# Performance work log

Measured on AMD Instinct MI355X. Metric: run time of the kernel, lower is better.

The kernel has to match this reference:

```python
import jax, jax.numpy as jnp
import numpy as np
import math

NUM_HEADS = 8
WINDOW_SIZE = 1025
GLOBAL_TOKENS = 512  # effectively min(4, GLOBAL_TOKENS) indices are used, as in the torch code


def setup_inputs() -> dict:
    key = jax.random.key(0)
    k0, k1, k2 = jax.random.split(key, 3)
    B, C, H, W = 2, 256, 64, 64
    x = jax.random.normal(k0, (B, C, H, W), dtype=jnp.float32)
    # proj1: Linear(C, 3C); proj2: Linear(C, C). Stored as [in, out] matrices.
    w1 = jax.random.normal(k1, (C, 3 * C), dtype=jnp.float32) * 0.02
    b1 = jnp.zeros((3 * C,), dtype=jnp.float32)
    w2 = jax.random.normal(k2, (C, C), dtype=jnp.float32) * 0.02
    b2 = jnp.zeros((C,), dtype=jnp.float32)
    return {"x": x, "w1": w1, "b1": b1, "w2": w2, "b2": b2}


def _longformer_bias(L, W, window_size, global_tokens, dtype):
    # band: |i - j| <= window_size // 2  (matches start/end loop in torch code)
    i = jnp.arange(L)
    band = jnp.abs(i[:, None] - i[None, :]) <= (window_size // 2)
    gidx = [0, W - 1, L - W, L - 1][:global_tokens]
    g = jnp.zeros((L,), dtype=bool).at[jnp.array(gidx)].set(True)
    mask = band | g[:, None] | g[None, :]
    return jnp.where(mask, jnp.array(0.0, dtype), jnp.array(-jnp.inf, dtype))


def reference(x, w1, b1, w2, b2):
    B, C, H, W = x.shape
    L = H * W
    hd = C // NUM_HEADS
    # b c h w -> b (h w) c
    xt = x.reshape(B, C, L).transpose(0, 2, 1)
    qkv = xt @ w1 + b1  # [B, L, 3C]
    # 'b L (C H K)' with K=3, H=heads: last dim factors as (head_dim, heads, 3)
    qkv = qkv.reshape(B, L, hd, NUM_HEADS, 3).transpose(4, 0, 3, 1, 2)  # [3, B, Hh, L, hd]
    q, k, v = qkv[0], qkv[1], qkv[2]
    bias = _longformer_bias(L, W, WINDOW_SIZE, GLOBAL_TOKENS, x.dtype)
    scale = math.sqrt(hd)
    attn = jnp.einsum('bhqc,bhkc->bhqk', q, k) / scale + bias
    attn = jax.nn.softmax(attn, axis=-1)
    o = jnp.einsum('bhqk,bhkc->bhqc', attn, v)  # [B, Hh, L, hd]
    # 'b H (h w) C -> b h w (C H)': channel index = c*num_heads + head
    o = o.transpose(0, 2, 3, 1).reshape(B, H, W, hd * NUM_HEADS)
    out = o @ w2 + b2  # [B, H, W, C]
    return out.transpose(0, 3, 1, 2)  # b h w C -> b C h w
```

## Files before the change

kernel.cpp:

```cpp
#include <hip/hip_runtime.h>
#include <hip/hip_bf16.h>

#define BB 2
#define CC 256
#define HEADS 8
#define HD 32
#define LL 4096
#define HALF_WIN 512

using short8  = __attribute__((ext_vector_type(8))) short;
using short4v = __attribute__((ext_vector_type(4))) short;
using float4v = __attribute__((ext_vector_type(4))) float;

__device__ __forceinline__ ushort f2bf(float x) {
    uint u = __float_as_uint(x);
    u += 0x7fff + ((u >> 16) & 1);
    return (ushort)(u >> 16);
}
__device__ __forceinline__ float ubf(ushort u) {
    return __uint_as_float((uint)u << 16);
}
__device__ __forceinline__ uint pk2bf(float a, float b) {
#if __has_builtin(__builtin_amdgcn_cvt_pk_bf16_f32)
    typedef __bf16 v2bf __attribute__((ext_vector_type(2)));
    union { v2bf v; uint u; } cv;
    cv.v = __builtin_amdgcn_cvt_pk_bf16_f32(a, b);
    return cv.u;
#else
    return (uint)f2bf(a) | ((uint)f2bf(b) << 16);
#endif
}
__device__ __forceinline__ float rexp2(float x) {
#if __has_builtin(__builtin_amdgcn_exp2f)
    return __builtin_amdgcn_exp2f(x);
#else
    return exp2f(x);
#endif
}

#define QSCALE 0.25503485f

__global__ __launch_bounds__(256) void wt_kernel(const float* __restrict__ w1,
                                                 const float* __restrict__ w2,
                                                 ushort* __restrict__ w1t,
                                                 ushort* __restrict__ w2t) {
    __shared__ float tl[16][17];
    const int tx = threadIdx.x & 15, ty = threadIdx.x >> 4;
    const int ci0 = blockIdx.x * 16;
    const int y = blockIdx.y;
    if (y < 48) {
        int j0 = y * 16;
        tl[ty][tx] = w1[(size_t)(ci0 + ty) * 768 + j0 + tx];
        __syncthreads();
        w1t[(size_t)(j0 + ty) * CC + ci0 + tx] = f2bf(tl[tx][ty]);
    } else {
        int co0 = (y - 48) * 16;
        tl[ty][tx] = w2[(size_t)(ci0 + ty) * CC + co0 + tx];
        __syncthreads();
        w2t[(size_t)(co0 + ty) * CC + ci0 + tx] = f2bf(tl[tx][ty]);
    }
}

__global__ __launch_bounds__(256) void qkv_kernel(const float* __restrict__ x,
                                                  const ushort* __restrict__ w1t,
                                                  const float* __restrict__ b1,
                                                  ushort* __restrict__ qb,
                                                  ushort* __restrict__ kb,
                                                  ushort* __restrict__ vt) {
    __shared__ __align__(16) ushort xs[32 * 264];
    const int dg = blockIdx.x;
    const int l0 = blockIdx.y * 32;
    const int b  = blockIdx.z;
    const int t  = threadIdx.x;
    const int w  = t >> 6, ln = t & 63, c = ln & 15, g = ln >> 4;

    {
        const int l  = t & 31;
        const int cG = (t >> 5) * 4;
#pragma unroll
        for (int p = 0; p < 8; p++) {
            int c0 = p * 32 + cG;
            float a0 = x[((size_t)b * CC + c0 + 0) * LL + l0 + l];
            float a1 = x[((size_t)b * CC + c0 + 1) * LL + l0 + l];
            float a2 = x[((size_t)b * CC + c0 + 2) * LL + l0 + l];
            float a3 = x[((size_t)b * CC + c0 + 3) * LL + l0 + l];
            uint2 u;
            u.x = pk2bf(a0, a1);
            u.y = pk2bf(a2, a3);
            *(uint2*)&xs[l * 264 + c0] = u;
        }
    }
    __syncthreads();

    const int jbase = dg * 192 + w * 48;
    float4v acc[3][2] = {};
#pragma unroll
    for (int ks = 0; ks < 8; ks++) {
        short8 af[3], bfr[2];
#pragma unroll
        for (int jt = 0; jt < 3; jt++)
            af[jt] = *(const short8*)(w1t + (size_t)(jbase + jt * 16 + c) * CC + ks * 32 + g * 8);
#pragma unroll
        for (int lt = 0; lt < 2; lt++)
            bfr[lt] = *(const short8*)&xs[(lt * 16 + c) * 264 + ks * 32 + g * 8];
#pragma unroll
        for (int jt = 0; jt < 3; jt++)
#pragma unroll
            for (int lt = 0; lt < 2; lt++)
                acc[jt][lt] = __builtin_amdgcn_mfma_f32_16x16x32_bf16(af[jt], bfr[lt], acc[jt][lt], 0, 0, 0);
    }
    __syncthreads();

    ushort* qs  = xs;
    ushort* ksm = xs + 32 * 72;
    ushort* vs  = xs + 2 * 32 * 72;

#pragma unroll
    for (int jt = 0; jt < 3; jt++) {
#pragma unroll
        for (int r = 0; r < 4; r++) {
            int j = jbase + jt * 16 + g * 4 + r;
            float bias = b1[j];
            int t3 = j % 3, h = (j / 3) & 7, dl = (j / 24) & 7;
            int slot = h * 8 + dl;
            float v0 = acc[jt][0][r] + bias;
            float v1 = acc[jt][1][r] + bias;
            if (t3 == 0) { v0 *= QSCALE; v1 *= QSCALE; }
            uint u01 = pk2bf(v0, v1);
            ushort* dst = (t3 == 0) ? qs : (t3 == 1) ? ksm : vs;
            int stride = (t3 == 2) ? 74 : 72;
            dst[c * stride + slot]        = (ushort)u01;
            dst[(16 + c) * stride + slot] = (ushort)(u01 >> 16);
        }
    }
    __syncthreads();

    {
        const int l = t & 31;
        const int h = t >> 5;
        size_t rowq = (((size_t)(b * 8 + h) * 4 + dg) * LL + l0 + l) * 8;
        *(short8*)(qb + rowq) = *(const short8*)&qs[l * 72 + h * 8];
        *(short8*)(kb + rowq) = *(const short8*)&ksm[l * 72 + h * 8];
#pragma unroll
        for (int p = 0; p < 8; p++) {
            int hd = p * 8 + h;
            vt[((size_t)(b * 8 + (hd >> 3)) * HD + dg * 8 + (hd & 7)) * LL + l0 + l] = vs[l * 74 + hd];
        }
    }
}

__device__ __forceinline__ int gcol_of(int tt) {
    return (tt == 0) ? 0 : (tt == 3) ? 63 : (tt == 252) ? LL - 64 : (tt == 255) ? LL - 1 : -1;
}

__global__ __launch_bounds__(256) void attn_kernel(const ushort* __restrict__ qb,
                                                   const ushort* __restrict__ kb,
                                                   const ushort* __restrict__ vt,
                                                   ushort* __restrict__ obuf,
                                                   float* __restrict__ gpart) {
    __shared__ __align__(16) char smem[27648];
    const int n = blockIdx.x;
    const int t = threadIdx.x;

    if (n < 256) {
        float* qs = (float*)smem;
        float* sc = qs + 128;
        const int bh = ((n & 7) << 1) | ((n >> 3) & 1);
        const int ch = n >> 4;
        const int gidx[4] = {0, 63, LL - 64, LL - 1};

        if (t < 128) {
            int r = t >> 5, dd = t & 31;
            int i = gidx[r];
            qs[r * 32 + dd] = ubf(qb[(((size_t)bh * 4 + (dd >> 3)) * LL + i) * 8 + (dd & 7)]);
        }
        __syncthreads();

        const int j = ch * 256 + t;
        float dot[4] = {};
#pragma unroll
        for (int s = 0; s < 4; s++) {
            const short8 kf = *(const short8*)(kb + (((size_t)bh * 4 + s) * LL + j) * 8);
#pragma unroll
            for (int e = 0; e < 8; e++) {
                float kv = ubf((ushort)kf[e]);
#pragma unroll
                for (int r = 0; r < 4; r++) dot[r] += qs[r * 32 + s * 8 + e] * kv;
            }
        }
#pragma unroll
        for (int r = 0; r < 4; r++) sc[r * 256 + t] = rexp2(dot[r]);
        __syncthreads();

        const int w = t >> 6, ln = t & 63;
        float den = sc[w * 256 + ln] + sc[w * 256 + ln + 64] +
                    sc[w * 256 + ln + 128] + sc[w * 256 + ln + 192];
#pragma unroll
        for (int o = 1; o < 64; o <<= 1) den += __shfl_xor(den, o);

        const int dd = ln & 31, half = ln >> 5;
        float acc = 0.f;
        const ushort* vrow = vt + ((size_t)bh * HD + dd) * LL + ch * 256 + half * 128;
#pragma unroll
        for (int q8 = 0; q8 < 16; q8++) {
            const short8 v8 = *(const short8*)(vrow + q8 * 8);
#pragma unroll
            for (int e = 0; e < 8; e++) acc += sc[w * 256 + half * 128 + q8 * 8 + e] * ubf((ushort)v8[e]);
        }
        acc += __shfl_xor(acc, 32);

        float* gp = gpart + (((size_t)bh * 16 + ch) * 4 + w) * 33;
        if (ln < 32) gp[dd] = acc;
        if (ln == 0) gp[32] = den;
        return;
    }

    ushort* pshare = (ushort*)smem;
    float*  cbuf   = (float*)smem;
    const int nb = n - 256;
    const int bh = ((nb & 7) << 1) | ((nb >> 3) & 1);
    const int it = nb >> 4;
    const int i0 = it * 64;
    const int w  = t >> 6;
    const int ln = t & 63;
    const int c  = ln & 15;
    const int g  = ln >> 4;

    const size_t slab = ((size_t)bh * 4 + g) * LL;

    short8 qf[4];
#pragma unroll
    for (int s = 0; s < 4; s++)
        qf[s] = *(const short8*)(qb + (slab + i0 + s * 16 + c) * 8);

    float4v o0[4], o1[4];
#pragma unroll
    for (int s = 0; s < 4; s++) {
#pragma unroll
        for (int r = 0; r < 4; r++) { o0[s][r] = 0.f; o1[s][r] = 0.f; }
    }
    float dsum[4] = {0.f, 0.f, 0.f, 0.f};

    int t0 = it * 4 - 32; if (t0 < 0) t0 = 0;
    int t1 = it * 4 + 35; if (t1 > 255) t1 = 255;
    int tf0 = it * 4 - 28; if (tf0 < 0) tf0 = 0;
    int tf1 = it * 4 + 31; if (tf1 > 255) tf1 = 255;

    int ml[12], nm = 0;
    for (int tt = t0; tt < tf0; tt++) ml[nm++] = tt;
    for (int tt = tf1 + 1; tt <= t1; tt++) ml[nm++] = tt;
    const int gt[4] = {0, 3, 252, 255};
#pragma unroll
    for (int e = 0; e < 4; e++)
        if (gt[e] < t0 || gt[e] > t1) ml[nm++] = gt[e];

    const ushort* vb = vt + (size_t)bh * HD * LL;
    ushort* wbb = pshare + w * 4 * 576;

    const int npair_f = (tf1 - tf0 + 1) >> 1;
    const int qq = npair_f >> 2, rem = npair_f & 3;
    const int mstart = w * qq + (w < rem ? w : rem);
    const int mcount = qq + (w < rem ? 1 : 0);
    const int tfs = tf0 + 2 * mstart;

    const ushort* kp  = kb + (slab + (size_t)(tfs * 16 + c)) * 8;
    const ushort* vp0 = vb + (size_t)c * LL + tfs * 16 + g * 8;
    const ushort* vp1 = vp0 + 16 * LL;

    short8 kfA, kfB, v0f, v1f;
    if (mcount > 0) {
        kfA = *(const short8*)kp;
        kfB = *(const short8*)(kp + 128);
        v0f = *(const short8*)vp0;
        v1f = *(const short8*)vp1;
    }
    for (int m = 0; m < mcount; m++) {
        const int adv = (m + 1 < mcount) ? 1 : 0;
        const ushort* kp2  = kp  + adv * 256;
        const ushort* vp02 = vp0 + adv * 32;
        const ushort* vp12 = vp1 + adv * 32;
        const short8 kfA2 = *(const short8*)kp2;
        const short8 kfB2 = *(const short8*)(kp2 + 128);
        const short8 v0f2 = *(const short8*)vp02;
        const short8 v1f2 = *(const short8*)vp12;

        float4v zero = {0.f, 0.f, 0.f, 0.f};
#pragma unroll
        for (int s = 0; s < 4; s++) {
            float4v sA = __builtin_amdgcn_mfma_f32_16x16x32_bf16(kfA, qf[s], zero, 0, 0, 0);
            float4v sB = __builtin_amdgcn_mfma_f32_16x16x32_bf16(kfB, qf[s], zero, 0, 0, 0);
            float pA[4], pB[4];
#pragma unroll
            for (int r = 0; r < 4; r++) { pA[r] = rexp2(sA[r]); dsum[s] += pA[r]; }
#pragma unroll
            for (int r = 0; r < 4; r++) { pB[r] = rexp2(sB[r]); dsum[s] += pB[r]; }
            uint2 ua, ub2;
            ua.x  = pk2bf(pA[0], pA[1]);
            ua.y  = pk2bf(pA[2], pA[3]);
            ub2.x = pk2bf(pB[0], pB[1]);
            ub2.y = pk2bf(pB[2], pB[3]);
            ushort* wb = wbb + s * 576;
            *(uint2*)&wb[c * 36 + 4 * g]      = ua;
            *(uint2*)&wb[c * 36 + 16 + 4 * g] = ub2;
        }
#pragma unroll
        for (int s = 0; s < 4; s++) {
            const ushort* wb = wbb + s * 576;
            union { short8 s8; short4v s4[2]; } pu;
            pu.s4[0] = *(const short4v*)&wb[c * 36 + 8 * g];
            pu.s4[1] = *(const short4v*)&wb[c * 36 + 8 * g + 4];
            o0[s] = __builtin_amdgcn_mfma_f32_16x16x32_bf16(pu.s8, v0f, o0[s], 0, 0, 0);
            o1[s] = __builtin_amdgcn_mfma_f32_16x16x32_bf16(pu.s8, v1f, o1[s], 0, 0, 0);
        }
        kfA = kfA2; kfB = kfB2; v0f = v0f2; v1f = v1f2;
        kp = kp2; vp0 = vp02; vp1 = vp12;
    }

    for (int p = 0; p < (nm >> 1); p++) {
        if ((p & 3) != w) continue;
        const int tA = ml[2 * p], tB = ml[2 * p + 1];
        const int gA = gcol_of(tA), gB = gcol_of(tB);
        const short8 mkA = *(const short8*)(kb + (slab + (size_t)(tA * 16 + c)) * 8);
        const short8 mkB = *(const short8*)(kb + (slab + (size_t)(tB * 16 + c)) * 8);
        const int jv = (g < 2) ? tA * 16 + g * 8 : tB * 16 + (g - 2) * 8;
        const short8 mv0 = *(const short8*)(vb + (size_t)c * LL + jv);
        const short8 mv1 = *(const short8*)(vb + (size_t)(16 + c) * LL + jv);
        float4v zero = {0.f, 0.f, 0.f, 0.f};
#pragma unroll
        for (int s = 0; s < 4; s++) {
            const int i = i0 + s * 16 + c;
            float4v sA = __builtin_amdgcn_mfma_f32_16x16x32_bf16(mkA, qf[s], zero, 0, 0, 0);
            float4v sB = __builtin_amdgcn_mfma_f32_16x16x32_bf16(mkB, qf[s], zero, 0, 0, 0);
            float pA[4], pB[4];
#pragma unroll
            for (int r = 0; r < 4; r++) {
                int j = tA * 16 + g * 4 + r;
                bool ok = ((unsigned)(i - j + HALF_WIN) <= 2u * HALF_WIN) | (j == gA);
                pA[r] = ok ? rexp2(sA[r]) : 0.f;
                dsum[s] += pA[r];
            }
#pragma unroll
            for (int r = 0; r < 4; r++) {
                int j = tB * 16 + g * 4 + r;
                bool ok = ((unsigned)(i - j + HALF_WIN) <= 2u * HALF_WIN) | (j == gB);
                pB[r] = ok ? rexp2(sB[r]) : 0.f;
                dsum[s] += pB[r];
            }
            uint2 ua, ub2;
            ua.x  = pk2bf(pA[0], pA[1]);
            ua.y  = pk2bf(pA[2], pA[3]);
            ub2.x = pk2bf(pB[0], pB[1]);
            ub2.y = pk2bf(pB[2], pB[3]);
            ushort* wb = wbb + s * 576;
            *(uint2*)&wb[c * 36 + 4 * g]      = ua;
            *(uint2*)&wb[c * 36 + 16 + 4 * g] = ub2;
        }
#pragma unroll
        for (int s = 0; s < 4; s++) {
            const ushort* wb = wbb + s * 576;
            union { short8 s8; short4v s4[2]; } pu;
            pu.s4[0] = *(const short4v*)&wb[c * 36 + 8 * g];
            pu.s4[1] = *(const short4v*)&wb[c * 36 + 8 * g + 4];
            o0[s] = __builtin_amdgcn_mfma_f32_16x16x32_bf16(pu.s8, mv0, o0[s], 0, 0, 0);
            o1[s] = __builtin_amdgcn_mfma_f32_16x16x32_bf16(pu.s8, mv1, o1[s], 0, 0, 0);
        }
    }

    __syncthreads();
#pragma unroll
    for (int s = 0; s < 4; s++) {
        if (s == w) continue;
        float* cb = &cbuf[((s * 3 + ((w < s) ? w : w - 1)) * 64 + ln) * 9];
#pragma unroll
        for (int r = 0; r < 4; r++) { cb[r] = o0[s][r]; cb[4 + r] = o1[s][r]; }
        cb[8] = dsum[s];
    }
    __syncthreads();

    float4v O0 = o0[w], O1 = o1[w];
    float ds = dsum[w];
#pragma unroll
    for (int k = 0; k < 3; k++) {
        const float* cb = &cbuf[((w * 3 + k) * 64 + ln) * 9];
#pragma unroll
        for (int r = 0; r < 4; r++) { O0[r] += cb[r]; O1[r] += cb[4 + r]; }
        ds += cb[8];
    }

    ds += __shfl_xor(ds, 16);
    ds += __shfl_xor(ds, 32);

    const int b = bh >> 3, hh = bh & 7;
#pragma unroll
    for (int r = 0; r < 4; r++) {
        float dn = __shfl(ds, g * 4 + r);
        float inv = 1.0f / dn;
        int irow = i0 + w * 16 + g * 4 + r;
        size_t rowb = ((size_t)b * LL + irow) * CC;
        obuf[rowb + (size_t)c * 8 + hh]        = f2bf(O0[r] * inv);
        obuf[rowb + (size_t)(16 + c) * 8 + hh] = f2bf(O1[r] * inv);
    }
}

__global__ __launch_bounds__(128) void attn_global_combine(const float* __restrict__ gpart,
                                                           ushort* __restrict__ obuf) {
    const int bh = blockIdx.x;
    const int t  = threadIdx.x;
    const int r  = t >> 5, dd = t & 31;
    const int gidx[4] = {0, 63, LL - 64, LL - 1};
    float pv = 0.f, den = 0.f;
#pragma unroll
    for (int ch = 0; ch < 16; ch++) {
        const float* gp = gpart + (((size_t)bh * 16 + ch) * 4 + r) * 33;
        pv  += gp[dd];
        den += gp[32];
    }
    const int b = bh >> 3, hh = bh & 7, i = gidx[r];
    obuf[((size_t)b * LL + i) * CC + dd * 8 + hh] = f2bf(pv / den);
}

__global__ __launch_bounds__(256) void proj_kernel(const ushort* __restrict__ obuf,
                                                   const ushort* __restrict__ w2t,
                                                   const float* __restrict__ b2,
                                                   float* __restrict__ out) {
    const int co0 = blockIdx.x * 16;
    const int w   = threadIdx.x >> 6;
    const int l0  = blockIdx.y * 128 + (w >> 1) * 64;
    const int nfb = (w & 1) * 2;
    const int b   = blockIdx.z;
    const int ln  = threadIdx.x & 63;
    const int c   = ln & 15, g = ln >> 4;

    float4v acc[2] = {};
    const ushort* arow = w2t + (size_t)(co0 + c) * CC + g * 8;
    const ushort* brow = obuf + ((size_t)b * LL + l0 + c) * CC + g * 8;
#pragma unroll
    for (int ks = 0; ks < 8; ks++) {
        const short8 af = *(const short8*)(arow + ks * 32);
#pragma unroll
        for (int k = 0; k < 2; k++) {
            const short8 bf = *(const short8*)(brow + (size_t)(nfb + k) * 16 * CC + ks * 32);
            acc[k] = __builtin_amdgcn_mfma_f32_16x16x32_bf16(af, bf, acc[k], 0, 0, 0);
        }
    }
#pragma unroll
    for (int k = 0; k < 2; k++) {
#pragma unroll
        for (int r = 0; r < 4; r++) {
            int co = co0 + g * 4 + r;
            int l  = l0 + (nfb + k) * 16 + c;
            out[((size_t)b * CC + co) * LL + l] = acc[k][r] + b2[co];
        }
    }
}

extern "C" void kernel_launch(void* const* d_in, const int* in_sizes, int n_in,
                              void* d_out, int out_size, void* d_ws, size_t ws_size,
                              hipStream_t stream) {
    const float* x  = (const float*)d_in[0];
    const float* w1 = (const float*)d_in[1];
    const float* b1 = (const float*)d_in[2];
    const float* w2 = (const float*)d_in[3];
    const float* b2 = (const float*)d_in[4];
    float* out = (float*)d_out;

    const size_t QKE = (size_t)BB * HEADS * LL * HD;
    const size_t OBE = (size_t)BB * LL * CC;
    ushort* qb  = (ushort*)d_ws;
    ushort* kb  = qb + QKE;
    ushort* vt  = kb + QKE;
    ushort* ob  = vt + QKE;
    float*  gp  = (float*)(ob + OBE);
    ushort* w2t = (ushort*)(gp + 16 * 16 * 4 * 33);
    ushort* w1t = w2t + CC * CC;

    wt_kernel<<<dim3(16, 64), 256, 0, stream>>>(w1, w2, w1t, w2t);
    qkv_kernel<<<dim3(4, 128, 2), 256, 0, stream>>>(x, w1t, b1, qb, kb, vt);
    attn_kernel<<<dim3(1280), 256, 0, stream>>>(qb, kb, vt, ob, gp);
    attn_global_combine<<<dim3(16), 128, 0, stream>>>(gp, ob);
    proj_kernel<<<dim3(16, 32, 2), 256, 0, stream>>>(ob, w2t, b2, out);
}
```

Before: 138.5 us.

## Fuse all stages into one persistent kernel with atomic grid barriers

Merges the weight transpose, QKV projection, attention, global-token combine and output projection into one persistent kernel of 512 blocks. Each stage loops over its former grid, and stages are separated by atomic-counter grid barriers; a memset resets the counters each call. This removes the launch gaps between kernels, but it relies on all 512 blocks being co-resident (launch_bounds 256,2) to avoid deadlock. Each barrier also serializes the stages, so a slow block in one stage holds up every block before the next.

```diff
diff --git a/kernel.cpp b/kernel.cpp
--- a/kernel.cpp
+++ b/kernel.cpp
@@ -7,6 +7,7 @@
 #define HD 32
 #define LL 4096
 #define HALF_WIN 512
+#define NBLK 512u
 
 using short8  = __attribute__((ext_vector_type(8))) short;
 using short4v = __attribute__((ext_vector_type(4))) short;
@@ -40,127 +41,143 @@
 
 #define QSCALE 0.25503485f
 
-__global__ __launch_bounds__(256) void wt_kernel(const float* __restrict__ w1,
-                                                 const float* __restrict__ w2,
-                                                 ushort* __restrict__ w1t,
-                                                 ushort* __restrict__ w2t) {
-    __shared__ float tl[16][17];
-    const int tx = threadIdx.x & 15, ty = threadIdx.x >> 4;
-    const int ci0 = blockIdx.x * 16;
-    const int y = blockIdx.y;
-    if (y < 48) {
-        int j0 = y * 16;
-        tl[ty][tx] = w1[(size_t)(ci0 + ty) * 768 + j0 + tx];
-        __syncthreads();
-        w1t[(size_t)(j0 + ty) * CC + ci0 + tx] = f2bf(tl[tx][ty]);
-    } else {
-        int co0 = (y - 48) * 16;
-        tl[ty][tx] = w2[(size_t)(ci0 + ty) * CC + co0 + tx];
-        __syncthreads();
-        w2t[(size_t)(co0 + ty) * CC + ci0 + tx] = f2bf(tl[tx][ty]);
-    }
-}
-
-__global__ __launch_bounds__(256) void qkv_kernel(const float* __restrict__ x,
-                                                  const ushort* __restrict__ w1t,
-                                                  const float* __restrict__ b1,
-                                                  ushort* __restrict__ qb,
-                                                  ushort* __restrict__ kb,
-                                                  ushort* __restrict__ vt) {
-    __shared__ __align__(16) ushort xs[32 * 264];
-    const int dg = blockIdx.x;
-    const int l0 = blockIdx.y * 32;
-    const int b  = blockIdx.z;
-    const int t  = threadIdx.x;
-    const int w  = t >> 6, ln = t & 63, c = ln & 15, g = ln >> 4;
-
-    {
-        const int l  = t & 31;
-        const int cG = (t >> 5) * 4;
-#pragma unroll
-        for (int p = 0; p < 8; p++) {
-            int c0 = p * 32 + cG;
-            float a0 = x[((size_t)b * CC + c0 + 0) * LL + l0 + l];
-            float a1 = x[((size_t)b * CC + c0 + 1) * LL + l0 + l];
-            float a2 = x[((size_t)b * CC + c0 + 2) * LL + l0 + l];
-            float a3 = x[((size_t)b * CC + c0 + 3) * LL + l0 + l];
-            uint2 u;
-            u.x = pk2bf(a0, a1);
-            u.y = pk2bf(a2, a3);
-            *(uint2*)&xs[l * 264 + c0] = u;
-        }
-    }
-    __syncthreads();
-
-    const int jbase = dg * 192 + w * 48;
-    float4v acc[3][2] = {};
-#pragma unroll
-    for (int ks = 0; ks < 8; ks++) {
-        short8 af[3], bfr[2];
-#pragma unroll
-        for (int jt = 0; jt < 3; jt++)
-            af[jt] = *(const short8*)(w1t + (size_t)(jbase + jt * 16 + c) * CC + ks * 32 + g * 8);
-#pragma unroll
-        for (int lt = 0; lt < 2; lt++)
-            bfr[lt] = *(const short8*)&xs[(lt * 16 + c) * 264 + ks * 32 + g * 8];
-#pragma unroll
-        for (int jt = 0; jt < 3; jt++)
-#pragma unroll
-            for (int lt = 0; lt < 2; lt++)
-                acc[jt][lt] = __builtin_amdgcn_mfma_f32_16x16x32_bf16(af[jt], bfr[lt], acc[jt][lt], 0, 0, 0);
-    }
-    __syncthreads();
-
-    ushort* qs  = xs;
-    ushort* ksm = xs + 32 * 72;
-    ushort* vs  = xs + 2 * 32 * 72;
-
-#pragma unroll
-    for (int jt = 0; jt < 3; jt++) {
-#pragma unroll
-        for (int r = 0; r < 4; r++) {
-            int j = jbase + jt * 16 + g * 4 + r;
-            float bias = b1[j];
-            int t3 = j % 3, h = (j / 3) & 7, dl = (j / 24) & 7;
-            int slot = h * 8 + dl;
-            float v0 = acc[jt][0][r] + bias;
-            float v1 = acc[jt][1][r] + bias;
-            if (t3 == 0) { v0 *= QSCALE; v1 *= QSCALE; }
-            uint u01 = pk2bf(v0, v1);
-            ushort* dst = (t3 == 0) ? qs : (t3 == 1) ? ksm : vs;
-            int stride = (t3 == 2) ? 74 : 72;
-            dst[c * stride + slot]        = (ushort)u01;
-            dst[(16 + c) * stride + slot] = (ushort)(u01 >> 16);
-        }
-    }
-    __syncthreads();
-
-    {
-        const int l = t & 31;
-        const int h = t >> 5;
-        size_t rowq = (((size_t)(b * 8 + h) * 4 + dg) * LL + l0 + l) * 8;
-        *(short8*)(qb + rowq) = *(const short8*)&qs[l * 72 + h * 8];
-        *(short8*)(kb + rowq) = *(const short8*)&ksm[l * 72 + h * 8];
-#pragma unroll
-        for (int p = 0; p < 8; p++) {
-            int hd = p * 8 + h;
-            vt[((size_t)(b * 8 + (hd >> 3)) * HD + dg * 8 + (hd & 7)) * LL + l0 + l] = vs[l * 74 + hd];
-        }
-    }
-}
-
 __device__ __forceinline__ int gcol_of(int tt) {
     return (tt == 0) ? 0 : (tt == 3) ? 63 : (tt == 252) ? LL - 64 : (tt == 255) ? LL - 1 : -1;
 }
 
-__global__ __launch_bounds__(256) void attn_kernel(const ushort* __restrict__ qb,
-                                                   const ushort* __restrict__ kb,
-                                                   const ushort* __restrict__ vt,
-                                                   ushort* __restrict__ obuf,
-                                                   float* __restrict__ gpart) {
+__device__ __forceinline__ void gbar(uint* ctr, int t) {
+    __syncthreads();
+    __threadfence();
+    if (t == 0) {
+        atomicAdd(ctr, 1u);
+        while (atomicAdd(ctr, 0u) < NBLK) __builtin_amdgcn_s_sleep(8);
+    }
+    __syncthreads();
+    __threadfence();
+}
+
+__global__ __launch_bounds__(256, 2) void mega_kernel(
+        const float* __restrict__ x,
+        const float* __restrict__ w1,
+        const float* __restrict__ b1,
+        const float* __restrict__ w2,
+        const float* __restrict__ b2,
+        float* __restrict__ out,
+        ushort* __restrict__ qb,
+        ushort* __restrict__ kb,
+        ushort* __restrict__ vt,
+        ushort* __restrict__ obuf,
+        float* __restrict__ gpart,
+        ushort* __restrict__ w2t,
+        ushort* __restrict__ w1t,
+        uint* __restrict__ bar) {
     __shared__ __align__(16) char smem[27648];
     const int n = blockIdx.x;
     const int t = threadIdx.x;
+
+    for (int jb = n; jb < 1024; jb += 512) {
+        float* tl = (float*)smem;
+        const int tx = t & 15, ty = t >> 4;
+        const int ci0 = (jb & 15) * 16;
+        const int y = jb >> 4;
+        if (y < 48) {
+            int j0 = y * 16;
+            tl[ty * 17 + tx] = w1[(size_t)(ci0 + ty) * 768 + j0 + tx];
+            __syncthreads();
+            w1t[(size_t)(j0 + ty) * CC + ci0 + tx] = f2bf(tl[tx * 17 + ty]);
+        } else {
+            int co0 = (y - 48) * 16;
+            tl[ty * 17 + tx] = w2[(size_t)(ci0 + ty) * CC + co0 + tx];
+            __syncthreads();
+            w2t[(size_t)(co0 + ty) * CC + ci0 + tx] = f2bf(tl[tx * 17 + ty]);
+        }
+        __syncthreads();
+    }
+    gbar(bar + 0, t);
+
+    for (int jb = n; jb < 1024; jb += 512) {
+        ushort* xs = (ushort*)smem;
+        const int dg = jb & 3;
+        const int l0 = ((jb >> 2) & 127) * 32;
+        const int b  = jb >> 9;
+        const int w  = t >> 6, ln = t & 63, c = ln & 15, g = ln >> 4;
+
+        {
+            const int l  = t & 31;
+            const int cG = (t >> 5) * 4;
+#pragma unroll
+            for (int p = 0; p < 8; p++) {
+                int c0 = p * 32 + cG;
+                float a0 = x[((size_t)b * CC + c0 + 0) * LL + l0 + l];
+                float a1 = x[((size_t)b * CC + c0 + 1) * LL + l0 + l];
+                float a2 = x[((size_t)b * CC + c0 + 2) * LL + l0 + l];
+                float a3 = x[((size_t)b * CC + c0 + 3) * LL + l0 + l];
+                uint2 u;
+                u.x = pk2bf(a0, a1);
+                u.y = pk2bf(a2, a3);
+                *(uint2*)&xs[l * 264 + c0] = u;
+            }
+        }
+        __syncthreads();
+
+        const int jbase = dg * 192 + w * 48;
+        float4v acc[3][2] = {};
+#pragma unroll
+        for (int ks = 0; ks < 8; ks++) {
+            short8 af[3], bfr[2];
+#pragma unroll
+            for (int jt = 0; jt < 3; jt++)
+                af[jt] = *(const short8*)(w1t + (size_t)(jbase + jt * 16 + c) * CC + ks * 32 + g * 8);
+#pragma unroll
+            for (int lt = 0; lt < 2; lt++)
+                bfr[lt] = *(const short8*)&xs[(lt * 16 + c) * 264 + ks * 32 + g * 8];
+#pragma unroll
+            for (int jt = 0; jt < 3; jt++)
+#pragma unroll
+                for (int lt = 0; lt < 2; lt++)
+                    acc[jt][lt] = __builtin_amdgcn_mfma_f32_16x16x32_bf16(af[jt], bfr[lt], acc[jt][lt], 0, 0, 0);
+        }
+        __syncthreads();
+
+        ushort* qs  = xs;
+        ushort* ksm = xs + 32 * 72;
+        ushort* vs  = xs + 2 * 32 * 72;
+
+#pragma unroll
+        for (int jt = 0; jt < 3; jt++) {
+#pragma unroll
+            for (int r = 0; r < 4; r++) {
+                int j = jbase + jt * 16 + g * 4 + r;
+                float bias = b1[j];
+                int t3 = j % 3, h = (j / 3) & 7, dl = (j / 24) & 7;
+                int slot = h * 8 + dl;
+                float v0 = acc[jt][0][r] + bias;
+                float v1 = acc[jt][1][r] + bias;
+                if (t3 == 0) { v0 *= QSCALE; v1 *= QSCALE; }
+                uint u01 = pk2bf(v0, v1);
+                ushort* dst = (t3 == 0) ? qs : (t3 == 1) ? ksm : vs;
+                int stride = (t3 == 2) ? 74 : 72;
+                dst[c * stride + slot]        = (ushort)u01;
+                dst[(16 + c) * stride + slot] = (ushort)(u01 >> 16);
+            }
+        }
+        __syncthreads();
+
+        {
+            const int l = t & 31;
+            const int h = t >> 5;
+            size_t rowq = (((size_t)(b * 8 + h) * 4 + dg) * LL + l0 + l) * 8;
+            *(short8*)(qb + rowq) = *(const short8*)&qs[l * 72 + h * 8];
+            *(short8*)(kb + rowq) = *(const short8*)&ksm[l * 72 + h * 8];
+#pragma unroll
+            for (int p = 0; p < 8; p++) {
+                int hd = p * 8 + h;
+                vt[((size_t)(b * 8 + (hd >> 3)) * HD + dg * 8 + (hd & 7)) * LL + l0 + l] = vs[l * 74 + hd];
+            }
+        }
+        __syncthreads();
+    }
+    gbar(bar + 1, t);
 
     if (n < 256) {
         float* qs = (float*)smem;
@@ -212,244 +229,244 @@
         float* gp = gpart + (((size_t)bh * 16 + ch) * 4 + w) * 33;
         if (ln < 32) gp[dd] = acc;
         if (ln == 0) gp[32] = den;
-        return;
-    }
-
-    ushort* pshare = (ushort*)smem;
-    float*  cbuf   = (float*)smem;
-    const int nb = n - 256;
-    const int bh = ((nb & 7) << 1) | ((nb >> 3) & 1);
-    const int it = nb >> 4;
-    const int i0 = it * 64;
-    const int w  = t >> 6;
-    const int ln = t & 63;
-    const int c  = ln & 15;
-    const int g  = ln >> 4;
-
-    const size_t slab = ((size_t)bh * 4 + g) * LL;
-
-    short8 qf[4];
-#pragma unroll
-    for (int s = 0; s < 4; s++)
-        qf[s] = *(const short8*)(qb + (slab + i0 + s * 16 + c) * 8);
-
-    float4v o0[4], o1[4];
-#pragma unroll
-    for (int s = 0; s < 4; s++) {
-#pragma unroll
-        for (int r = 0; r < 4; r++) { o0[s][r] = 0.f; o1[s][r] = 0.f; }
-    }
-    float dsum[4] = {0.f, 0.f, 0.f, 0.f};
-
-    int t0 = it * 4 - 32; if (t0 < 0) t0 = 0;
-    int t1 = it * 4 + 35; if (t1 > 255) t1 = 255;
-    int tf0 = it * 4 - 28; if (tf0 < 0) tf0 = 0;
-    int tf1 = it * 4 + 31; if (tf1 > 255) tf1 = 255;
-
-    int ml[12], nm = 0;
-    for (int tt = t0; tt < tf0; tt++) ml[nm++] = tt;
-    for (int tt = tf1 + 1; tt <= t1; tt++) ml[nm++] = tt;
-    const int gt[4] = {0, 3, 252, 255};
-#pragma unroll
-    for (int e = 0; e < 4; e++)
-        if (gt[e] < t0 || gt[e] > t1) ml[nm++] = gt[e];
-
-    const ushort* vb = vt + (size_t)bh * HD * LL;
-    ushort* wbb = pshare + w * 4 * 576;
-
-    const int npair_f = (tf1 - tf0 + 1) >> 1;
-    const int qq = npair_f >> 2, rem = npair_f & 3;
-    const int mstart = w * qq + (w < rem ? w : rem);
-    const int mcount = qq + (w < rem ? 1 : 0);
-    const int tfs = tf0 + 2 * mstart;
-
-    const ushort* kp  = kb + (slab + (size_t)(tfs * 16 + c)) * 8;
-    const ushort* vp0 = vb + (size_t)c * LL + tfs * 16 + g * 8;
-    const ushort* vp1 = vp0 + 16 * LL;
-
-    short8 kfA, kfB, v0f, v1f;
-    if (mcount > 0) {
-        kfA = *(const short8*)kp;
-        kfB = *(const short8*)(kp + 128);
-        v0f = *(const short8*)vp0;
-        v1f = *(const short8*)vp1;
-    }
-    for (int m = 0; m < mcount; m++) {
-        const int adv = (m + 1 < mcount) ? 1 : 0;
-        const ushort* kp2  = kp  + adv * 256;
-        const ushort* vp02 = vp0 + adv * 32;
-        const ushort* vp12 = vp1 + adv * 32;
-        const short8 kfA2 = *(const short8*)kp2;
-        const short8 kfB2 = *(const short8*)(kp2 + 128);
-        const short8 v0f2 = *(const short8*)vp02;
-        const short8 v1f2 = *(const short8*)vp12;
-
-        float4v zero = {0.f, 0.f, 0.f, 0.f};
+        __syncthreads();
+    }
+
+    for (int jb = n; jb < 1024; jb += 512) {
+        ushort* pshare = (ushort*)smem;
+        float*  cbuf   = (float*)smem;
+        const int nb = jb;
+        const int bh = ((nb & 7) << 1) | ((nb >> 3) & 1);
+        const int it = nb >> 4;
+        const int i0 = it * 64;
+        const int w  = t >> 6;
+        const int ln = t & 63;
+        const int c  = ln & 15;
+        const int g  = ln >> 4;
+
+        const size_t slab = ((size_t)bh * 4 + g) * LL;
+
+        short8 qf[4];
+#pragma unroll
+        for (int s = 0; s < 4; s++)
+            qf[s] = *(const short8*)(qb + (slab + i0 + s * 16 + c) * 8);
+
+        float4v o0[4], o1[4];
 #pragma unroll
         for (int s = 0; s < 4; s++) {
-            float4v sA = __builtin_amdgcn_mfma_f32_16x16x32_bf16(kfA, qf[s], zero, 0, 0, 0);
-            float4v sB = __builtin_amdgcn_mfma_f32_16x16x32_bf16(kfB, qf[s], zero, 0, 0, 0);
-            float pA[4], pB[4];
-#pragma unroll
-            for (int r = 0; r < 4; r++) { pA[r] = rexp2(sA[r]); dsum[s] += pA[r]; }
-#pragma unroll
-            for (int r = 0; r < 4; r++) { pB[r] = rexp2(sB[r]); dsum[s] += pB[r]; }
-            uint2 ua, ub2;
-            ua.x  = pk2bf(pA[0], pA[1]);
-            ua.y  = pk2bf(pA[2], pA[3]);
-            ub2.x = pk2bf(pB[0], pB[1]);
-            ub2.y = pk2bf(pB[2], pB[3]);
-            ushort* wb = wbb + s * 576;
-            *(uint2*)&wb[c * 36 + 4 * g]      = ua;
-            *(uint2*)&wb[c * 36 + 16 + 4 * g] = ub2;
-        }
+#pragma unroll
+            for (int r = 0; r < 4; r++) { o0[s][r] = 0.f; o1[s][r] = 0.f; }
+        }
+        float dsum[4] = {0.f, 0.f, 0.f, 0.f};
+
+        int t0 = it * 4 - 32; if (t0 < 0) t0 = 0;
+        int t1 = it * 4 + 35; if (t1 > 255) t1 = 255;
+        int tf0 = it * 4 - 28; if (tf0 < 0) tf0 = 0;
+        int tf1 = it * 4 + 31; if (tf1 > 255) tf1 = 255;
+
+        int ml[12], nm = 0;
+        for (int tt = t0; tt < tf0; tt++) ml[nm++] = tt;
+        for (int tt = tf1 + 1; tt <= t1; tt++) ml[nm++] = tt;
+        const int gt[4] = {0, 3, 252, 255};
+#pragma unroll
+        for (int e = 0; e < 4; e++)
+            if (gt[e] < t0 || gt[e] > t1) ml[nm++] = gt[e];
+
+        const ushort* vb = vt + (size_t)bh * HD * LL;
+        ushort* wbb = pshare + w * 4 * 576;
+
+        const int npair_f = (tf1 - tf0 + 1) >> 1;
+        const int qq = npair_f >> 2, rem = npair_f & 3;
+        const int mstart = w * qq + (w < rem ? w : rem);
+        const int mcount = qq + (w < rem ? 1 : 0);
+        const int tfs = tf0 + 2 * mstart;
+
+        const ushort* kp  = kb + (slab + (size_t)(tfs * 16 + c)) * 8;
+        const ushort* vp0 = vb + (size_t)c * LL + tfs * 16 + g * 8;
+        const ushort* vp1 = vp0 + 16 * LL;
+
+        short8 kfA, kfB, v0f, v1f;
+        if (mcount > 0) {
+            kfA = *(const short8*)kp;
+            kfB = *(const short8*)(kp + 128);
+            v0f = *(const short8*)vp0;
+            v1f = *(const short8*)vp1;
+        }
+        for (int m = 0; m < mcount; m++) {
+            const int adv = (m + 1 < mcount) ? 1 : 0;
+            const ushort* kp2  = kp  + adv * 256;
+            const ushort* vp02 = vp0 + adv * 32;
+            const ushort* vp12 = vp1 + adv * 32;
+            const short8 kfA2 = *(const short8*)kp2;
+            const short8 kfB2 = *(const short8*)(kp2 + 128);
+            const short8 v0f2 = *(const short8*)vp02;
+            const short8 v1f2 = *(const short8*)vp12;
+
+            float4v zero = {0.f, 0.f, 0.f, 0.f};
+#pragma unroll
+            for (int s = 0; s < 4; s++) {
+                float4v sA = __builtin_amdgcn_mfma_f32_16x16x32_bf16(kfA, qf[s], zero, 0, 0, 0);
+                float4v sB = __builtin_amdgcn_mfma_f32_16x16x32_bf16(kfB, qf[s], zero, 0, 0, 0);
+                float pA[4], pB[4];
+#pragma unroll
+                for (int r = 0; r < 4; r++) { pA[r] = rexp2(sA[r]); dsum[s] += pA[r]; }
+#pragma unroll
+                for (int r = 0; r < 4; r++) { pB[r] = rexp2(sB[r]); dsum[s] += pB[r]; }
+                uint2 ua, ub2;
+                ua.x  = pk2bf(pA[0], pA[1]);
+                ua.y  = pk2bf(pA[2], pA[3]);
+                ub2.x = pk2bf(pB[0], pB[1]);
+                ub2.y = pk2bf(pB[2], pB[3]);
+                ushort* wb = wbb + s * 576;
+                *(uint2*)&wb[c * 36 + 4 * g]      = ua;
+                *(uint2*)&wb[c * 36 + 16 + 4 * g] = ub2;
+            }
+#pragma unroll
+            for (int s = 0; s < 4; s++) {
+                const ushort* wb = wbb + s * 576;
+                union { short8 s8; short4v s4[2]; } pu;
+                pu.s4[0] = *(const short4v*)&wb[c * 36 + 8 * g];
+                pu.s4[1] = *(const short4v*)&wb[c * 36 + 8 * g + 4];
+                o0[s] = __builtin_amdgcn_mfma_f32_16x16x32_bf16(pu.s8, v0f, o0[s], 0, 0, 0);
+                o1[s] = __builtin_amdgcn_mfma_f32_16x16x32_bf16(pu.s8, v1f, o1[s], 0, 0, 0);
+            }
+            kfA = kfA2; kfB = kfB2; v0f = v0f2; v1f = v1f2;
+            kp = kp2; vp0 = vp02; vp1 = vp12;
+        }
+
+        for (int p = 0; p < (nm >> 1); p++) {
+            if ((p & 3) != w) continue;
+            const int tA = ml[2 * p], tB = ml[2 * p + 1];
+            const int gA = gcol_of(tA), gB = gcol_of(tB);
+            const short8 mkA = *(const short8*)(kb + (slab + (size_t)(tA * 16 + c)) * 8);
+            const short8 mkB = *(const short8*)(kb + (slab + (size_t)(tB * 16 + c)) * 8);
+            const int jv = (g < 2) ? tA * 16 + g * 8 : tB * 16 + (g - 2) * 8;
+            const short8 mv0 = *(const short8*)(vb + (size_t)c * LL + jv);
+            const short8 mv1 = *(const short8*)(vb + (size_t)(16 + c) * LL + jv);
+            float4v zero = {0.f, 0.f, 0.f, 0.f};
+#pragma unroll
+            for (int s = 0; s < 4; s++) {
+                const int i = i0 + s * 16 + c;
+                float4v sA = __builtin_amdgcn_mfma_f32_16x16x32_bf16(mkA, qf[s], zero, 0, 0, 0);
+                float4v sB = __builtin_amdgcn_mfma_f32_16x16x32_bf16(mkB, qf[s], zero, 0, 0, 0);
+                float pA[4], pB[4];
+#pragma unroll
+                for (int r = 0; r < 4; r++) {
+                    int j = tA * 16 + g * 4 + r;
+                    bool ok = ((unsigned)(i - j + HALF_WIN) <= 2u * HALF_WIN) | (j == gA);
+                    pA[r] = ok ? rexp2(sA[r]) : 0.f;
+                    dsum[s] += pA[r];
+                }
+#pragma unroll
+                for (int r = 0; r < 4; r++) {
+                    int j = tB * 16 + g * 4 + r;
+                    bool ok = ((unsigned)(i - j + HALF_WIN) <= 2u * HALF_WIN) | (j == gB);
+                    pB[r] = ok ? rexp2(sB[r]) : 0.f;
+                    dsum[s] += pB[r];
+                }
+                uint2 ua, ub2;
+                ua.x  = pk2bf(pA[0], pA[1]);
+                ua.y  = pk2bf(pA[2], pA[3]);
+                ub2.x = pk2bf(pB[0], pB[1]);
+                ub2.y = pk2bf(pB[2], pB[3]);
+                ushort* wb = wbb + s * 576;
+                *(uint2*)&wb[c * 36 + 4 * g]      = ua;
+                *(uint2*)&wb[c * 36 + 16 + 4 * g] = ub2;
+            }
+#pragma unroll
+            for (int s = 0; s < 4; s++) {
+                const ushort* wb = wbb + s * 576;
+                union { short8 s8; short4v s4[2]; } pu;
+                pu.s4[0] = *(const short4v*)&wb[c * 36 + 8 * g];
+                pu.s4[1] = *(const short4v*)&wb[c * 36 + 8 * g + 4];
+                o0[s] = __builtin_amdgcn_mfma_f32_16x16x32_bf16(pu.s8, mv0, o0[s], 0, 0, 0);
+                o1[s] = __builtin_amdgcn_mfma_f32_16x16x32_bf16(pu.s8, mv1, o1[s], 0, 0, 0);
+            }
+        }
+
+        __syncthreads();
 #pragma unroll
         for (int s = 0; s < 4; s++) {
-            const ushort* wb = wbb + s * 576;
-            union { short8 s8; short4v s4[2]; } pu;
-            pu.s4[0] = *(const short4v*)&wb[c * 36 + 8 * g];
-            pu.s4[1] = *(const short4v*)&wb[c * 36 + 8 * g + 4];
-            o0[s] = __builtin_amdgcn_mfma_f32_16x16x32_bf16(pu.s8, v0f, o0[s], 0, 0, 0);
-            o1[s] = __builtin_amdgcn_mfma_f32_16x16x32_bf16(pu.s8, v1f, o1[s], 0, 0, 0);
-        }
-        kfA = kfA2; kfB = kfB2; v0f = v0f2; v1f = v1f2;
-        kp = kp2; vp0 = vp02; vp1 = vp12;
-    }
-
-    for (int p = 0; p < (nm >> 1); p++) {
-        if ((p & 3) != w) continue;
-        const int tA = ml[2 * p], tB = ml[2 * p + 1];
-        const int gA = gcol_of(tA), gB = gcol_of(tB);
-        const short8 mkA = *(const short8*)(kb + (slab + (size_t)(tA * 16 + c)) * 8);
-        const short8 mkB = *(const short8*)(kb + (slab + (size_t)(tB * 16 + c)) * 8);
-        const int jv = (g < 2) ? tA * 16 + g * 8 : tB * 16 + (g - 2) * 8;
-        const short8 mv0 = *(const short8*)(vb + (size_t)c * LL + jv);
-        const short8 mv1 = *(const short8*)(vb + (size_t)(16 + c) * LL + jv);
-        float4v zero = {0.f, 0.f, 0.f, 0.f};
-#pragma unroll
-        for (int s = 0; s < 4; s++) {
-            const int i = i0 + s * 16 + c;
-            float4v sA = __builtin_amdgcn_mfma_f32_16x16x32_bf16(mkA, qf[s], zero, 0, 0, 0);
-            float4v sB = __builtin_amdgcn_mfma_f32_16x16x32_bf16(mkB, qf[s], zero, 0, 0, 0);
-            float pA[4], pB[4];
+            if (s == w) continue;
+            float* cb = &cbuf[((s * 3 + ((w < s) ? w : w - 1)) * 64 + ln) * 9];
+#pragma unroll
+            for (int r = 0; r < 4; r++) { cb[r] = o0[s][r]; cb[4 + r] = o1[s][r]; }
+            cb[8] = dsum[s];
+        }
+        __syncthreads();
+
+        float4v O0 = o0[w], O1 = o1[w];
+        float ds = dsum[w];
+#pragma unroll
+        for (int k = 0; k < 3; k++) {
+            const float* cb = &cbuf[((w * 3 + k) * 64 + ln) * 9];
+#pragma unroll
+            for (int r = 0; r < 4; r++) { O0[r] += cb[r]; O1[r] += cb[4 + r]; }
+            ds += cb[8];
+        }
+
+        ds += __shfl_xor(ds, 16);
+        ds += __shfl_xor(ds, 32);
+
+        const int b = bh >> 3, hh = bh & 7;
+#pragma unroll
+        for (int r = 0; r < 4; r++) {
+            float dn = __shfl(ds, g * 4 + r);
+            float inv = 1.0f / dn;
+            int irow = i0 + w * 16 + g * 4 + r;
+            size_t rowb = ((size_t)b * LL + irow) * CC;
+            obuf[rowb + (size_t)c * 8 + hh]        = f2bf(O0[r] * inv);
+            obuf[rowb + (size_t)(16 + c) * 8 + hh] = f2bf(O1[r] * inv);
+        }
+        __syncthreads();
+    }
+    gbar(bar + 2, t);
+
+    if (n < 16 && t < 128) {
+        const int bh = n;
+        const int r  = t >> 5, dd = t & 31;
+        const int gidx[4] = {0, 63, LL - 64, LL - 1};
+        float pv = 0.f, den = 0.f;
+#pragma unroll
+        for (int ch = 0; ch < 16; ch++) {
+            const float* gp = gpart + (((size_t)bh * 16 + ch) * 4 + r) * 33;
+            pv  += gp[dd];
+            den += gp[32];
+        }
+        const int b = bh >> 3, hh = bh & 7, i = gidx[r];
+        obuf[((size_t)b * LL + i) * CC + dd * 8 + hh] = f2bf(pv / den);
+    }
+    gbar(bar + 3, t);
+
+    for (int jb = n; jb < 1024; jb += 512) {
+        const int co0 = (jb & 15) * 16;
+        const int w   = t >> 6;
+        const int l0  = ((jb >> 4) & 31) * 128 + (w >> 1) * 64;
+        const int nfb = (w & 1) * 2;
+        const int b   = jb >> 9;
+        const int ln  = t & 63;
+        const int c   = ln & 15, g = ln >> 4;
+
+        float4v acc[2] = {};
+        const ushort* arow = w2t + (size_t)(co0 + c) * CC + g * 8;
+        const ushort* brow = obuf + ((size_t)b * LL + l0 + c) * CC + g * 8;
+#pragma unroll
+        for (int ks = 0; ks < 8; ks++) {
+            const short8 af = *(const short8*)(arow + ks * 32);
+#pragma unroll
+            for (int k = 0; k < 2; k++) {
+                const short8 bf = *(const short8*)(brow + (size_t)(nfb + k) * 16 * CC + ks * 32);
+                acc[k] = __builtin_amdgcn_mfma_f32_16x16x32_bf16(af, bf, acc[k], 0, 0, 0);
+            }
+        }
+#pragma unroll
+        for (int k = 0; k < 2; k++) {
 #pragma unroll
             for (int r = 0; r < 4; r++) {
-                int j = tA * 16 + g * 4 + r;
-                bool ok = ((unsigned)(i - j + HALF_WIN) <= 2u * HALF_WIN) | (j == gA);
-                pA[r] = ok ? rexp2(sA[r]) : 0.f;
-                dsum[s] += pA[r];
-            }
-#pragma unroll
-            for (int r = 0; r < 4; r++) {
-                int j = tB * 16 + g * 4 + r;
-                bool ok = ((unsigned)(i - j + HALF_WIN) <= 2u * HALF_WIN) | (j == gB);
-                pB[r] = ok ? rexp2(sB[r]) : 0.f;
-                dsum[s] += pB[r];
-            }
-            uint2 ua, ub2;
-            ua.x  = pk2bf(pA[0], pA[1]);
-            ua.y  = pk2bf(pA[2], pA[3]);
-            ub2.x = pk2bf(pB[0], pB[1]);
-            ub2.y = pk2bf(pB[2], pB[3]);
-            ushort* wb = wbb + s * 576;
-            *(uint2*)&wb[c * 36 + 4 * g]      = ua;
-            *(uint2*)&wb[c * 36 + 16 + 4 * g] = ub2;
-        }
-#pragma unroll
-        for (int s = 0; s < 4; s++) {
-            const ushort* wb = wbb + s * 576;
-            union { short8 s8; short4v s4[2]; } pu;
-            pu.s4[0] = *(const short4v*)&wb[c * 36 + 8 * g];
-            pu.s4[1] = *(const short4v*)&wb[c * 36 + 8 * g + 4];
-            o0[s] = __builtin_amdgcn_mfma_f32_16x16x32_bf16(pu.s8, mv0, o0[s], 0, 0, 0);
-            o1[s] = __builtin_amdgcn_mfma_f32_16x16x32_bf16(pu.s8, mv1, o1[s], 0, 0, 0);
-        }
-    }
-
-    __syncthreads();
-#pragma unroll
-    for (int s = 0; s < 4; s++) {
-        if (s == w) continue;
-        float* cb = &cbuf[((s * 3 + ((w < s) ? w : w - 1)) * 64 + ln) * 9];
-#pragma unroll
-        for (int r = 0; r < 4; r++) { cb[r] = o0[s][r]; cb[4 + r] = o1[s][r]; }
-        cb[8] = dsum[s];
-    }
-    __syncthreads();
-
-    float4v O0 = o0[w], O1 = o1[w];
-    float ds = dsum[w];
-#pragma unroll
-    for (int k = 0; k < 3; k++) {
-        const float* cb = &cbuf[((w * 3 + k) * 64 + ln) * 9];
-#pragma unroll
-        for (int r = 0; r < 4; r++) { O0[r] += cb[r]; O1[r] += cb[4 + r]; }
-        ds += cb[8];
-    }
-
-    ds += __shfl_xor(ds, 16);
-    ds += __shfl_xor(ds, 32);
-
-    const int b = bh >> 3, hh = bh & 7;
-#pragma unroll
-    for (int r = 0; r < 4; r++) {
-        float dn = __shfl(ds, g * 4 + r);
-        float inv = 1.0f / dn;
-        int irow = i0 + w * 16 + g * 4 + r;
-        size_t rowb = ((size_t)b * LL + irow) * CC;
-        obuf[rowb + (size_t)c * 8 + hh]        = f2bf(O0[r] * inv);
-        obuf[rowb + (size_t)(16 + c) * 8 + hh] = f2bf(O1[r] * inv);
-    }
-}
-
-__global__ __launch_bounds__(128) void attn_global_combine(const float* __restrict__ gpart,
-                                                           ushort* __restrict__ obuf) {
-    const int bh = blockIdx.x;
-    const int t  = threadIdx.x;
-    const int r  = t >> 5, dd = t & 31;
-    const int gidx[4] = {0, 63, LL - 64, LL - 1};
-    float pv = 0.f, den = 0.f;
-#pragma unroll
-    for (int ch = 0; ch < 16; ch++) {
-        const float* gp = gpart + (((size_t)bh * 16 + ch) * 4 + r) * 33;
-        pv  += gp[dd];
-        den += gp[32];
-    }
-    const int b = bh >> 3, hh = bh & 7, i = gidx[r];
-    obuf[((size_t)b * LL + i) * CC + dd * 8 + hh] = f2bf(pv / den);
-}
-
-__global__ __launch_bounds__(256) void proj_kernel(const ushort* __restrict__ obuf,
-                                                   const ushort* __restrict__ w2t,
-                                                   const float* __restrict__ b2,
-                                                   float* __restrict__ out) {
-    const int co0 = blockIdx.x * 16;
-    const int w   = threadIdx.x >> 6;
-    const int l0  = blockIdx.y * 128 + (w >> 1) * 64;
-    const int nfb = (w & 1) * 2;
-    const int b   = blockIdx.z;
-    const int ln  = threadIdx.x & 63;
-    const int c   = ln & 15, g = ln >> 4;
-
-    float4v acc[2] = {};
-    const ushort* arow = w2t + (size_t)(co0 + c) * CC + g * 8;
-    const ushort* brow = obuf + ((size_t)b * LL + l0 + c) * CC + g * 8;
-#pragma unroll
-    for (int ks = 0; ks < 8; ks++) {
-        const short8 af = *(const short8*)(arow + ks * 32);
-#pragma unroll
-        for (int k = 0; k < 2; k++) {
-            const short8 bf = *(const short8*)(brow + (size_t)(nfb + k) * 16 * CC + ks * 32);
-            acc[k] = __builtin_amdgcn_mfma_f32_16x16x32_bf16(af, bf, acc[k], 0, 0, 0);
-        }
-    }
-#pragma unroll
-    for (int k = 0; k < 2; k++) {
-#pragma unroll
-        for (int r = 0; r < 4; r++) {
-            int co = co0 + g * 4 + r;
-            int l  = l0 + (nfb + k) * 16 + c;
-            out[((size_t)b * CC + co) * LL + l] = acc[k][r] + b2[co];
+                int co = co0 + g * 4 + r;
+                int l  = l0 + (nfb + k) * 16 + c;
+                out[((size_t)b * CC + co) * LL + l] = acc[k][r] + b2[co];
+            }
         }
     }
 }
@@ -473,10 +490,9 @@
     float*  gp  = (float*)(ob + OBE);
     ushort* w2t = (ushort*)(gp + 16 * 16 * 4 * 33);
     ushort* w1t = w2t + CC * CC;
-
-    wt_kernel<<<dim3(16, 64), 256, 0, stream>>>(w1, w2, w1t, w2t);
-    qkv_kernel<<<dim3(4, 128, 2), 256, 0, stream>>>(x, w1t, b1, qb, kb, vt);
-    attn_kernel<<<dim3(1280), 256, 0, stream>>>(qb, kb, vt, ob, gp);
-    attn_global_combine<<<dim3(16), 128, 0, stream>>>(gp, ob);
-    proj_kernel<<<dim3(16, 32, 2), 256, 0, stream>>>(ob, w2t, b2, out);
-}
+    uint*   bar = (uint*)(w1t + 768 * CC);
+
+    hipMemsetAsync(bar, 0, 4 * sizeof(uint), stream);
+    mega_kernel<<<dim3(NBLK), dim3(256), 0, stream>>>(
+        x, w1, b1, w2, b2, out, qb, kb, vt, ob, gp, w2t, w1t, bar);
+}
```

After: 515.9 us. 273% more time.
